# Kernel tuning notes

Measured on AMD Instinct MI355X. Metric: run time of the kernel, lower is better.

Reference implementation:

```python
import jax, jax.numpy as jnp
import numpy as np

H = 2048   # hidden_size
NH = 16    # num_heads
D = 128    # head_dim_qk == head_dim_v
K = 4      # conv_kernel_size


def _causal_depthwise_conv(x, w, b):
    # x: [B,S,C], w: [C,K], b: [C]. Matches torch Conv1d(groups=C, padding=K-1)[..., :S]
    S = x.shape[1]
    xp = jnp.pad(x, ((0, 0), (K - 1, 0), (0, 0)))
    y = b
    for j in range(K):
        y = y + xp[:, j:j + S, :] * w[:, j]
    return y


def setup_inputs() -> dict:
    key = jax.random.key(0)
    ks = jax.random.split(key, 18)
    s = 0.02
    B, S = 2, 2048
    return {
        "x": jax.random.normal(ks[0], (B, S, H), dtype=jnp.float32),
        "Wq": jax.random.normal(ks[1], (H, NH * D), dtype=jnp.float32) * s,
        "Wk": jax.random.normal(ks[2], (H, NH * D), dtype=jnp.float32) * s,
        "Wv": jax.random.normal(ks[3], (H, NH * D), dtype=jnp.float32) * s,
        "Wa": jax.random.normal(ks[4], (H, NH), dtype=jnp.float32) * s,
        "ba": jax.random.normal(ks[5], (NH,), dtype=jnp.float32) * s,
        "Wb": jax.random.normal(ks[6], (H, NH), dtype=jnp.float32) * s,
        "bb": jax.random.normal(ks[7], (NH,), dtype=jnp.float32) * s,
        "Wg": jax.random.normal(ks[8], (H, NH * D), dtype=jnp.float32) * s,
        "Wo": jax.random.normal(ks[9], (NH * D, H), dtype=jnp.float32) * s,
        "qcw": jax.random.normal(ks[10], (NH * D, K), dtype=jnp.float32) * s,
        "qcb": jax.random.normal(ks[11], (NH * D,), dtype=jnp.float32) * s,
        "kcw": jax.random.normal(ks[12], (NH * D, K), dtype=jnp.float32) * s,
        "kcb": jax.random.normal(ks[13], (NH * D,), dtype=jnp.float32) * s,
        "vcw": jax.random.normal(ks[14], (NH * D, K), dtype=jnp.float32) * s,
        "vcb": jax.random.normal(ks[15], (NH * D,), dtype=jnp.float32) * s,
        "ln_w": jnp.ones((D,), dtype=jnp.float32),
        "ln_b": jnp.zeros((D,), dtype=jnp.float32),
    }


def _forward(x, Wq, Wk, Wv, Wa, ba, Wb, bb, Wg, Wo,
             qcw, qcb, kcw, kcb, vcw, vcb, ln_w, ln_b):
    B, S, _ = x.shape
    q = _causal_depthwise_conv(x @ Wq, qcw, qcb)
    k = _causal_depthwise_conv(x @ Wk, kcw, kcb)
    v = _causal_depthwise_conv(x @ Wv, vcw, vcb)
    q = jax.nn.silu(q).reshape(B, S, NH, D)
    k = jax.nn.silu(k).reshape(B, S, NH, D) * (D ** -0.5)
    v = jax.nn.silu(v).reshape(B, S, NH, D)
    alpha = jax.nn.sigmoid(x @ Wa + ba)  # [B,S,NH]
    beta = jax.nn.sigmoid(x @ Wb + bb)   # [B,S,NH]

    # time-major for scan
    qt = jnp.moveaxis(q, 1, 0)       # [S,B,NH,D]
    kt = jnp.moveaxis(k, 1, 0)
    vt = jnp.moveaxis(v, 1, 0)
    at = jnp.moveaxis(alpha, 1, 0)   # [S,B,NH]
    bt = jnp.moveaxis(beta, 1, 0)

    def step(St, inp):
        q_, k_, v_, a_, b_ = inp
        sk = jnp.einsum('bhij,bhj->bhi', St, k_)            # [B,NH,D]
        err = sk - v_
        Sn = (a_[..., None, None] * St
              - b_[..., None, None] * err[..., None] * k_[..., None, :])
        o_ = jnp.einsum('bhij,bhj->bhi', Sn, q_)
        return Sn, o_

    S0 = jnp.zeros((B, NH, D, D), dtype=x.dtype)
    _, o = jax.lax.scan(step, S0, (qt, kt, vt, at, bt))
    o = jnp.moveaxis(o, 0, 1)  # [B,S,NH,D]

    # LayerNorm over head_dim
    mu = jnp.mean(o, axis=-1, keepdims=True)
    var = jnp.mean(jnp.square(o - mu), axis=-1, keepdims=True)
    o = (o - mu) * jax.lax.rsqrt(var + 1e-5) * ln_w + ln_b

    g = jax.nn.sigmoid(x @ Wg).reshape(B, S, NH, D)
    o = (o * g).reshape(B, S, NH * D)
    return o @ Wo


def reference(x, Wq, Wk, Wv, Wa, ba, Wb, bb, Wg, Wo,
              qcw, qcb, kcw, kcb, vcw, vcb, ln_w, ln_b):
    return _forward(x, Wq, Wk, Wv, Wa, ba, Wb, bb, Wg, Wo,
                    qcw, qcb, kcw, kcb, vcw, vcb, ln_w, ln_b)
```

## Files before the change

### kernel.cpp

```cpp
#include <hip/hip_runtime.h>
#include <math.h>
#include <stdint.h>

typedef unsigned short u16;
typedef unsigned int u32;
typedef __attribute__((ext_vector_type(8))) short short8;
typedef __attribute__((ext_vector_type(4))) float f32x4;

#define MFMA16(a, b, c) __builtin_amdgcn_mfma_f32_16x16x32_bf16(a, b, c, 0, 0, 0)

__device__ __forceinline__ u16 f2bf(float f) {
  union { float f; u32 u; } v; v.f = f;
  return (u16)((v.u + 0x7FFFu + ((v.u >> 16) & 1u)) >> 16);
}
__device__ __forceinline__ float bf2f(u16 h) {
  union { u32 u; float f; } v; v.u = ((u32)h) << 16; return v.f;
}
__device__ __forceinline__ float bflo(u32 p) {
  union { u32 u; float f; } v; v.u = p << 16; return v.f;
}
__device__ __forceinline__ float bfhi(u32 p) {
  union { u32 u; float f; } v; v.u = p & 0xffff0000u; return v.f;
}
__device__ __forceinline__ float sigm(float x) { return 1.f / (1.f + expf(-x)); }

__global__ void k_cvt_x(const float* __restrict__ x, u16* __restrict__ xb) {
  int i = (blockIdx.x * 256 + threadIdx.x) * 8;
  float4 a = *(const float4*)(x + i);
  float4 b = *(const float4*)(x + i + 4);
  uint4 p;
  p.x = (u32)f2bf(a.x) | ((u32)f2bf(a.y) << 16);
  p.y = (u32)f2bf(a.z) | ((u32)f2bf(a.w) << 16);
  p.z = (u32)f2bf(b.x) | ((u32)f2bf(b.y) << 16);
  p.w = (u32)f2bf(b.z) | ((u32)f2bf(b.w) << 16);
  *(uint4*)(xb + i) = p;
}

__global__ void k_tconv(const float* __restrict__ W, u16* __restrict__ Wt) {
  __shared__ float tile[32][33];
  int n0 = blockIdx.x * 32, k0 = blockIdx.y * 32;
  int tc = threadIdx.x & 31, tr = threadIdx.x >> 5;
  #pragma unroll
  for (int p = 0; p < 4; ++p) {
    int k = k0 + p * 8 + tr;
    tile[p * 8 + tr][tc] = W[(size_t)k * 2048 + n0 + tc];
  }
  __syncthreads();
  #pragma unroll
  for (int p = 0; p < 4; ++p) {
    int n = n0 + p * 8 + tr;
    Wt[(size_t)n * 2048 + k0 + tc] = f2bf(tile[tc][p * 8 + tr]);
  }
}

__global__ void k_tconv4(const float* __restrict__ W0, const float* __restrict__ W1,
                         const float* __restrict__ W2, const float* __restrict__ W3,
                         u16* __restrict__ Wt) {
  __shared__ float tile[32][33];
  int z = blockIdx.z;
  const float* W = (z == 0) ? W0 : (z == 1) ? W1 : (z == 2) ? W2 : W3;
  u16* dst = Wt + (size_t)z * 2048 * 2048;
  int n0 = blockIdx.x * 32, k0 = blockIdx.y * 32;
  int tc = threadIdx.x & 31, tr = threadIdx.x >> 5;
  #pragma unroll
  for (int p = 0; p < 4; ++p) {
    int k = k0 + p * 8 + tr;
    tile[p * 8 + tr][tc] = W[(size_t)k * 2048 + n0 + tc];
  }
  __syncthreads();
  #pragma unroll
  for (int p = 0; p < 4; ++p) {
    int n = n0 + p * 8 + tr;
    dst[(size_t)n * 2048 + k0 + tc] = f2bf(tile[tc][p * 8 + tr]);
  }
}

__device__ __forceinline__ void gld_lds16(const u16* g, u16* l) {
  __builtin_amdgcn_global_load_lds((const __attribute__((address_space(1))) void*)g,
                                   (__attribute__((address_space(3))) void*)l, 16, 0, 0);
}

template <int MODE>
__global__ void k_gemm(const u16* __restrict__ A, const u16* __restrict__ Bw,
                       void* C0, void* C1, int Kd) {
  __shared__ u16 As[2][128 * 32];
  __shared__ u16 Bs[2][128 * 32];
  const int t = threadIdx.x;
  const int lane = t & 63, wv = t >> 6;
  const int wr = wv >> 1, wc = wv & 1;
  const int m0 = blockIdx.y * 128, n0 = blockIdx.x * 128;
  f32x4 acc[4][4] = {};
  const int NT = Kd / 32;

  auto stage = [&](int buf, int kt) {
    #pragma unroll
    for (int i = 0; i < 2; ++i) {
      int li = i * 256 + t;
      int row = li >> 2, kc = li & 3;
      const u16* ga = A + (size_t)(m0 + row) * Kd + kt * 32 + kc * 8;
      gld_lds16(ga, &As[buf][(i * 256 + wv * 64) * 8]);
      const u16* gb = Bw + (size_t)(n0 + row) * Kd + kt * 32 + kc * 8;
      gld_lds16(gb, &Bs[buf][(i * 256 + wv * 64) * 8]);
    }
  };

  stage(0, 0);
  __syncthreads();
  int buf = 0;
  const int l15 = lane & 15, l4 = lane >> 4;
  for (int kt = 0; kt < NT; ++kt) {
    if (kt + 1 < NT) stage(buf ^ 1, kt + 1);
    short8 af[4], bfr[4];
    #pragma unroll
    for (int m = 0; m < 4; ++m)
      af[m] = *(const short8*)&As[buf][(wr * 64 + m * 16 + l15) * 32 + l4 * 8];
    #pragma unroll
    for (int n = 0; n < 4; ++n)
      bfr[n] = *(const short8*)&Bs[buf][(wc * 64 + n * 16 + l15) * 32 + l4 * 8];
    #pragma unroll
    for (int m = 0; m < 4; ++m)
      #pragma unroll
      for (int n = 0; n < 4; ++n)
        acc[m][n] = MFMA16(af[m], bfr[n], acc[m][n]);
    __syncthreads();
    buf ^= 1;
  }
  #pragma unroll
  for (int m = 0; m < 4; ++m)
    #pragma unroll
    for (int n = 0; n < 4; ++n)
      #pragma unroll
      for (int e = 0; e < 4; ++e) {
        int row = m0 + wr * 64 + m * 16 + l4 * 4 + e;
        int col = n0 + wc * 64 + n * 16 + l15;
        if (MODE == 0) {
          ((float*)C0)[(size_t)row * 2048 + col] = acc[m][n][e];
        } else {
          u16 vb = f2bf(acc[m][n][e]);
          if (n0 < 6144) ((u16*)C0)[(size_t)row * 6144 + col] = vb;
          else           ((u16*)C1)[(size_t)row * 2048 + (col - 6144)] = vb;
        }
      }
}

template <int MODE>
__global__ __launch_bounds__(512)
void k_gemm8(const u16* __restrict__ A, const u16* __restrict__ Bw,
             void* C0, void* C1) {
  __shared__ u16 lds[65536];
  const int t = threadIdx.x;
  const int w = t >> 6, lane = t & 63;
  const int l15 = lane & 15, l4 = lane >> 4;
  const int wm = w >> 2, wn = w & 3;
  const int m0 = blockIdx.y * 256, n0 = blockIdx.x * 256;

  f32x4 acc[8][4] = {};
  short8 a[4][2], b[4][2];

  auto stageHalf = [&](int buf, int kt, int mat, int half) {
    const u16* src = mat ? Bw : A;
    const int row0 = (mat ? n0 : m0) + half * 128;
    u16* dst0 = &lds[mat * 32768 + (buf * 2 + half) * 8192 + w * 1024];
    #pragma unroll
    for (int i = 0; i < 2; ++i) {
      int f = w * 128 + i * 64 + lane;
      int rr = f >> 3, g = f & 7;
      const u16* ga = src + (size_t)(row0 + rr) * 2048 + kt * 64 + ((g ^ (rr & 7)) << 3);
      gld_lds16(ga, dst0 + i * 512);
    }
  };
  auto rdA = [&](int buf, int mq, int ks) {
    int row = wm * 64 + (mq & 3) * 16 + l15;
    int g = (l4 + ks * 4) ^ (row & 7);
    return *(const short8*)&lds[(buf * 2 + (mq >> 2)) * 8192 + row * 64 + g * 8];
  };
  auto rdB = [&](int buf, int n, int ks) {
    int row = wn * 32 + (n & 1) * 16 + l15;
    int g = (l4 + ks * 4) ^ (row & 7);
    return *(const short8*)&lds[32768 + (buf * 2 + (n >> 1)) * 8192 + row * 64 + g * 8];
  };

  stageHalf(0, 0, 0, 0); stageHalf(0, 0, 1, 0);
  stageHalf(0, 0, 1, 1); stageHalf(0, 0, 0, 1);
  asm volatile("s_waitcnt vmcnt(0)" ::: "memory");
  __builtin_amdgcn_s_barrier();
  __builtin_amdgcn_sched_barrier(0);

  for (int kt = 0; kt < 32; ++kt) {
    const int bufc = kt & 1, bufn = bufc ^ 1;
    const int ktn = (kt + 1 < 32) ? kt + 1 : 31;

    #pragma unroll
    for (int mq = 0; mq < 4; ++mq) { a[mq][0] = rdA(bufc, mq, 0); a[mq][1] = rdA(bufc, mq, 1); }
    #pragma unroll
    for (int n = 0; n < 2; ++n) { b[n][0] = rdB(bufc, n, 0); b[n][1] = rdB(bufc, n, 1); }
    stageHalf(bufn, ktn, 0, 0);
    __builtin_amdgcn_s_barrier();
    asm volatile("s_waitcnt lgkmcnt(0)" ::: "memory");
    __builtin_amdgcn_sched_barrier(0);
    __builtin_amdgcn_s_setprio(1);
    #pragma unroll
    for (int mq = 0; mq < 4; ++mq)
      #pragma unroll
      for (int n = 0; n < 2; ++n) {
        acc[mq][n] = MFMA16(a[mq][0], b[n][0], acc[mq][n]);
        acc[mq][n] = MFMA16(a[mq][1], b[n][1], acc[mq][n]);
      }
    __builtin_amdgcn_s_setprio(0);
    asm volatile("s_waitcnt vmcnt(4)" ::: "memory");
    __builtin_amdgcn_s_barrier();
    __builtin_amdgcn_sched_barrier(0);

    #pragma unroll
    for (int n = 2; n < 4; ++n) { b[n][0] = rdB(bufc, n, 0); b[n][1] = rdB(bufc, n, 1); }
    stageHalf(bufn, ktn, 1, 0);
    __builtin_amdgcn_s_barrier();
    asm volatile("s_waitcnt lgkmcnt(0)" ::: "memory");
    __builtin_amdgcn_sched_barrier(0);
    __builtin_amdgcn_s_setprio(1);
    #pragma unroll
    for (int mq = 0; mq < 4; ++mq)
      #pragma unroll
      for (int n = 2; n < 4; ++n) {
        acc[mq][n] = MFMA16(a[mq][0], b[n][0], acc[mq][n]);
        acc[mq][n] = MFMA16(a[mq][1], b[n][1], acc[mq][n]);
      }
    __builtin_amdgcn_s_setprio(0);
    asm volatile("s_waitcnt vmcnt(4)" ::: "memory");
    __builtin_amdgcn_s_barrier();
    __builtin_amdgcn_sched_barrier(0);

    #pragma unroll
    for (int mq = 0; mq < 4; ++mq) { a[mq][0] = rdA(bufc, mq + 4, 0); a[mq][1] = rdA(bufc, mq + 4, 1); }
    stageHalf(bufn, ktn, 1, 1);
    __builtin_amdgcn_s_barrier();
    asm volatile("s_waitcnt lgkmcnt(0)" ::: "memory");
    __builtin_amdgcn_sched_barrier(0);
    __builtin_amdgcn_s_setprio(1);
    #pragma unroll
    for (int mq = 0; mq < 4; ++mq)
      #pragma unroll
      for (int n = 2; n < 4; ++n) {
        acc[mq + 4][n] = MFMA16(a[mq][0], b[n][0], acc[mq + 4][n]);
        acc[mq + 4][n] = MFMA16(a[mq][1], b[n][1], acc[mq + 4][n]);
      }
    __builtin_amdgcn_s_setprio(0);
    __builtin_amdgcn_s_barrier();
    __builtin_amdgcn_sched_barrier(0);

    stageHalf(bufn, ktn, 0, 1);
    __builtin_amdgcn_s_barrier();
    asm volatile("s_waitcnt lgkmcnt(0)" ::: "memory");
    __builtin_amdgcn_sched_barrier(0);
    __builtin_amdgcn_s_setprio(1);
    #pragma unroll
    for (int mq = 0; mq < 4; ++mq)
      #pragma unroll
      for (int n = 0; n < 2; ++n) {
        acc[mq + 4][n] = MFMA16(a[mq][0], b[n][0], acc[mq + 4][n]);
        acc[mq + 4][n] = MFMA16(a[mq][1], b[n][1], acc[mq + 4][n]);
      }
    __builtin_amdgcn_s_setprio(0);
    asm volatile("s_waitcnt vmcnt(4)" ::: "memory");
    __builtin_amdgcn_s_barrier();
    __builtin_amdgcn_sched_barrier(0);
  }

  const bool toG = (MODE == 1) && (n0 >= 6144);
  #pragma unroll
  for (int mq = 0; mq < 8; ++mq) {
    int row = m0 + (mq >> 2) * 128 + wm * 64 + (mq & 3) * 16 + l4 * 4;
    #pragma unroll
    for (int n = 0; n < 4; ++n) {
      int col = n0 + (n >> 1) * 128 + wn * 32 + (n & 1) * 16 + l15;
      #pragma unroll
      for (int e = 0; e < 4; ++e) {
        if (MODE == 0) {
          ((float*)C0)[(size_t)(row + e) * 2048 + col] = acc[mq][n][e];
        } else {
          u16 vb = f2bf(acc[mq][n][e]);
          if (!toG) ((u16*)C0)[(size_t)(row + e) * 6144 + col] = vb;
          else      ((u16*)C1)[(size_t)(row + e) * 2048 + (col - 6144)] = vb;
        }
      }
    }
  }
}

__global__ void k_ab(const float* __restrict__ x, const float* __restrict__ Wa,
                     const float* __restrict__ ba, const float* __restrict__ Wb,
                     const float* __restrict__ bb, float* __restrict__ ab2) {
  int t = threadIdx.x;
  int col = t & 31, lr = t >> 5;
  int rowi = blockIdx.x * 8 + lr;
  const float* W = (col < 16) ? Wa : Wb;
  int c = col & 15;
  float acc = 0.f;
  const float* xr = x + (size_t)rowi * 2048;
  for (int k = 0; k < 2048; k += 4) {
    float4 xv = *(const float4*)(xr + k);
    acc += xv.x * W[(k + 0) * 16 + c] + xv.y * W[(k + 1) * 16 + c] +
           xv.z * W[(k + 2) * 16 + c] + xv.w * W[(k + 3) * 16 + c];
  }
  acc += (col < 16) ? ba[c] : bb[c];
  float sg = sigm(acc);
  int b = rowi >> 11, s = rowi & 2047;
  size_t base = ((size_t)(b * 16 + c) * 2048 + s) * 2;
  if (col < 16) ab2[base + 0] = sg;
  else          ab2[base + 1] = sg;
}

__global__ void k_conv(const u16* __restrict__ projQKV,
                       const float* __restrict__ qcw, const float* __restrict__ qcb,
                       const float* __restrict__ kcw, const float* __restrict__ kcb,
                       const float* __restrict__ vcw, const float* __restrict__ vcb,
                       u16* __restrict__ qkv2) {
  int idx = blockIdx.x * 256 + threadIdx.x;
  int cq = idx % 1536, rrow = idx / 1536;
  int c = cq * 4;
  int s = rrow & 2047, b = rrow >> 11;
  int type = c >> 11;
  int ch = c & 2047;
  int h = ch >> 7, d = ch & 127;
  const float* cw; const float* cb;
  if (type == 0)      { cw = qcw; cb = qcb; }
  else if (type == 1) { cw = kcw; cb = kcb; }
  else                { cw = vcw; cb = vcb; }
  float wch[4][4];
  #pragma unroll
  for (int u = 0; u < 4; ++u) {
    float4 wv = *(const float4*)(cw + (ch + u) * 4);
    wch[u][0] = wv.x; wch[u][1] = wv.y; wch[u][2] = wv.z; wch[u][3] = wv.w;
  }
  float4 bv = *(const float4*)(cb + ch);
  float accv[4] = {bv.x, bv.y, bv.z, bv.w};
  #pragma unroll
  for (int j = 0; j < 4; ++j) {
    int sj = s - 3 + j;
    if (sj < 0) continue;
    const u16* p = projQKV + (size_t)(rrow + j - 3) * 6144 + c;
    u32 pa = *(const u32*)p;
    u32 pb = *(const u32*)(p + 2);
    accv[0] += bflo(pa) * wch[0][j];
    accv[1] += bfhi(pa) * wch[1][j];
    accv[2] += bflo(pb) * wch[2][j];
    accv[3] += bfhi(pb) * wch[3][j];
  }
  u16 o4[4];
  #pragma unroll
  for (int u = 0; u < 4; ++u) {
    float y = accv[u];
    float sv = y * sigm(y);
    if (type == 1) sv *= 0.08838834764831845f;
    o4[u] = f2bf(sv);
  }
  int off = (type == 1 ? 0 : (type == 0 ? 128 : 256)) + d;
  u16* dst = qkv2 + ((size_t)(b * 16 + h) * 2048 + s) * 384 + off;
  *(u32*)dst       = (u32)o4[0] | ((u32)o4[1] << 16);
  *(u32*)(dst + 2) = (u32)o4[2] | ((u32)o4[3] << 16);
}

__global__ __launch_bounds__(256)
void k_chunkA(const u16* __restrict__ qkv2, const float* __restrict__ ab2,
              u16* __restrict__ Tbv, u16* __restrict__ nTbk,
              u16* __restrict__ Aq, float* __restrict__ vecs,
              u16* __restrict__ Kt) {
  __shared__ u16 Kl[64][136], Ql[64][136];
  __shared__ float Gk[4096], Gq[4096];
  __shared__ float clL[64], laL[64], bL[64], gpL[64];
  const int unit = blockIdx.x;
  const int bh = unit >> 5, c = unit & 31;
  const int t = threadIdx.x;
  const int wv = t >> 6, lane = t & 63;
  const int l15 = lane & 15, l4 = lane >> 4;
  const u16* qb = qkv2 + ((size_t)bh * 2048 + c * 64) * 384;

  #pragma unroll
  for (int p = 0; p < 4; ++p) {
    int ld = p * 256 + t;
    int row = ld >> 4, c8 = (ld & 15) * 8;
    *(uint4*)&Kl[row][c8] = *(const uint4*)(qb + (size_t)row * 384 + c8);
    *(uint4*)&Ql[row][c8] = *(const uint4*)(qb + (size_t)row * 384 + 128 + c8);
  }
  if (wv == 0) {
    float2 abv = *(const float2*)(ab2 + ((size_t)bh * 2048 + c * 64 + lane) * 2);
    float la = log2f(abv.x);
    float cl = la;
    #pragma unroll
    for (int o = 1; o < 64; o <<= 1) {
      float nv = __shfl_up(cl, o, 64);
      if (lane >= o) cl += nv;
    }
    clL[lane] = cl; laL[lane] = la; bL[lane] = abv.y;
    gpL[lane] = exp2f(cl - la);
  }
  __syncthreads();

  {
    const int t0 = (wv >> 1) * 32, i0 = (wv & 1) * 32;
    f32x4 ak[2][2] = {}, aq[2][2] = {};
    #pragma unroll
    for (int ks = 0; ks < 4; ++ks) {
      short8 bk[2], Ka[2], Qa[2];
      #pragma unroll
      for (int n = 0; n < 2; ++n)
        bk[n] = *(const short8*)&Kl[i0 + n * 16 + l15][ks * 32 + l4 * 8];
      #pragma unroll
      for (int m = 0; m < 2; ++m) {
        Ka[m] = *(const short8*)&Kl[t0 + m * 16 + l15][ks * 32 + l4 * 8];
        Qa[m] = *(const short8*)&Ql[t0 + m * 16 + l15][ks * 32 + l4 * 8];
      }
      #pragma unroll
      for (int m = 0; m < 2; ++m)
        #pragma unroll
        for (int n = 0; n < 2; ++n) {
          ak[m][n] = MFMA16(Ka[m], bk[n], ak[m][n]);
          aq[m][n] = MFMA16(Qa[m], bk[n], aq[m][n]);
        }
    }
    #pragma unroll
    for (int m = 0; m < 2; ++m)
      #pragma unroll
      for (int n = 0; n < 2; ++n)
        #pragma unroll
        for (int e = 0; e < 4; ++e) {
          int row = t0 + m * 16 + l4 * 4 + e;
          int col = i0 + n * 16 + l15;
          Gk[row * 64 + col] = ak[m][n][e];
          Gq[row * 64 + col] = aq[m][n][e];
        }
  }
  __syncthreads();

  #pragma unroll
  for (int p = 0; p < 16; ++p) {
    int e = p * 256 + t; int tt = e >> 6, ii = e & 63;
    float lv = 0.f;
    if (ii < tt) lv = bL[tt] * Gk[e] * exp2f(clL[tt] - laL[tt] - clL[ii]);
    float av = (ii <= tt) ? Gq[e] * exp2f(clL[tt] - clL[ii]) : 0.f;
    Gk[e] = lv;
    Aq[(size_t)unit * 4096 + e] = f2bf(av);
  }
  __syncthreads();

  float X[64];
  if (t < 128) {
    #pragma unroll
    for (int r = 0; r < 64; ++r)
      X[r] = bL[r] * bf2f(qb[(size_t)r * 384 + 256 + t]);
  } else {
    int ck = t - 128;
    #pragma unroll
    for (int r = 0; r < 64; ++r)
      X[r] = -bL[r] * gpL[r] * bf2f(Kl[r][ck]);
  }
  #pragma unroll
  for (int i = 0; i < 63; ++i) {
    float xi = X[i];
    #pragma unroll
    for (int r = i + 1; r < 64; ++r)
      X[r] = fmaf(-Gk[r * 64 + i], xi, X[r]);
  }
  if (t < 128) {
    #pragma unroll
    for (int r = 0; r < 64; ++r)
      Tbv[(size_t)unit * 8192 + r * 128 + t] = f2bf(X[r]);
  } else {
    #pragma unroll
    for (int r = 0; r < 64; ++r)
      nTbk[(size_t)unit * 8192 + r * 128 + (t - 128)] = f2bf(X[r]);
  }
  if (t < 64) {
    vecs[(size_t)unit * 128 + t] = exp2f(clL[t]);
    vecs[(size_t)unit * 128 + 64 + t] = exp2f(clL[63] - clL[t]);
  }
  {
    int dk = t >> 1, tt0 = (t & 1) * 32;
    uint4 w[4];
    u16* wp = (u16*)w;
    #pragma unroll
    for (int j = 0; j < 32; ++j) wp[j] = Kl[tt0 + j][dk];
    uint4* dst = (uint4*)(Kt + (size_t)unit * 8192 + dk * 64 + tt0);
    dst[0] = w[0]; dst[1] = w[1]; dst[2] = w[2]; dst[3] = w[3];
  }
}

#define OFF_NT  0
#define OFF_AQ  8192
#define OFF_Q   12288
#define OFF_KT  20480
#define OFF_TBV 28672
#define STG_U16 29696

__global__ __launch_bounds__(256)
void k_chunkB(const u16* __restrict__ qkv2, const u16* __restrict__ Tbv,
              const u16* __restrict__ nTbk, const u16* __restrict__ Aq,
              const u16* __restrict__ Kt, const float* __restrict__ vecs,
              float* __restrict__ o) {
  __shared__ u16 stg[2][STG_U16];
  __shared__ float S[16 * 132];
  __shared__ u16 Ut[16 * 72], Utd[16 * 72];
  __shared__ float gdl[2][128];
  const int bid = blockIdx.x;
  const int xcd = bid & 7, within = bid >> 3;
  const int sl = within & 7, hgrp = within >> 3;
  const int bh = hgrp * 8 + xcd;
  const int dv0 = sl * 16;
  const int b = bh >> 4, h = bh & 15;
  const int t = threadIdx.x;
  const int wv = t >> 6, lane = t & 63;
  const int l15 = lane & 15, l4 = lane >> 4;
  const int t0 = wv * 16;
  const int dk0 = wv * 32;
  const u16* qbase = qkv2 + (size_t)bh * 2048 * 384;
  float* obase = o + (size_t)b * 2048 * 2048 + h * 128 + dv0;

  for (int p = t; p < 16 * 132; p += 256) S[p] = 0.f;

  auto stage = [&](int buf, int c) {
    u16* sb = &stg[buf][0];
    const size_t unit = (size_t)bh * 32 + c;
    const u16* tbk = nTbk + unit * 8192;
    const u16* aqp = Aq + unit * 4096;
    const u16* ktp = Kt + unit * 8192;
    const u16* tbv = Tbv + unit * 8192;
    const u16* qp  = qbase + (size_t)c * 64 * 384 + 128;
    #pragma unroll
    for (int r = 0; r < 4; ++r) {
      int f = r * 256 + t; int rr = f >> 4, c16 = f & 15;
      gld_lds16(tbk + rr * 128 + (c16 ^ (rr & 7)) * 8, sb + OFF_NT + (r * 256 + wv * 64) * 8);
    }
    #pragma unroll
    for (int r = 0; r < 2; ++r) {
      int f = r * 256 + t; int rr = f >> 3, c8 = f & 7;
      gld_lds16(aqp + rr * 64 + (c8 ^ (rr & 7)) * 8, sb + OFF_AQ + (r * 256 + wv * 64) * 8);
    }
    #pragma unroll
    for (int r = 0; r < 4; ++r) {
      int f = r * 256 + t; int rr = f >> 4, c16 = f & 15;
      gld_lds16(qp + rr * 384 + (c16 ^ (rr & 7)) * 8, sb + OFF_Q + (r * 256 + wv * 64) * 8);
    }
    #pragma unroll
    for (int r = 0; r < 4; ++r) {
      int f = r * 256 + t; int rr = f >> 3, c8 = f & 7;
      gld_lds16(ktp + rr * 64 + (c8 ^ (rr & 7)) * 8, sb + OFF_KT + (r * 256 + wv * 64) * 8);
    }
    if (t < 128)
      gld_lds16(tbv + (t >> 1) * 128 + dv0 + (t & 1) * 8, sb + OFF_TBV + wv * 64 * 8);
  };

  stage(0, 0);
  if (t < 128) gdl[0][t] = vecs[(size_t)bh * 32 * 128 + t];
  __syncthreads();

  for (int c = 0; c < 32; ++c) {
    const int buf = c & 1;
    const u16* sb = &stg[buf][0];
    float vnext = 0.f;
    if (c + 1 < 32) {
      stage(buf ^ 1, c + 1);
      if (t < 128) vnext = vecs[((size_t)bh * 32 + c + 1) * 128 + t];
    }

    f32x4 acc1 = {}, acc2 = {};
    #pragma unroll
    for (int e = 0; e < 4; ++e)
      acc1[e] = bf2f(sb[OFF_TBV + (t0 + l4 * 4 + e) * 16 + l15]);
    #pragma unroll
    for (int ks = 0; ks < 4; ++ks) {
      short8 bhi, blo;
      {
        const float* srow = &S[l15 * 132 + ks * 32 + l4 * 8];
        float4 s0 = *(const float4*)srow, s1 = *(const float4*)(srow + 4);
        float sv[8] = {s0.x, s0.y, s0.z, s0.w, s1.x, s1.y, s1.z, s1.w};
        #pragma unroll
        for (int j = 0; j < 8; ++j) {
          u16 hv = f2bf(sv[j]);
          bhi[j] = (short)hv;
          blo[j] = (short)f2bf(sv[j] - bf2f(hv));
        }
      }
      const int cx = ((ks * 4 + l4) ^ (l15 & 7)) * 8;
      short8 a1 = *(const short8*)&sb[OFF_NT + (t0 + l15) * 128 + cx];
      short8 a2 = *(const short8*)&sb[OFF_Q + (t0 + l15) * 128 + cx];
      acc1 = MFMA16(a1, bhi, acc1);
      acc1 = MFMA16(a1, blo, acc1);
      acc2 = MFMA16(a2, bhi, acc2);
      acc2 = MFMA16(a2, blo, acc2);
    }
    {
      u16 up[4], ud[4];
      #pragma unroll
      for (int e = 0; e < 4; ++e) {
        float uv = acc1[e];
        up[e] = f2bf(uv);
        ud[e] = f2bf(uv * gdl[buf][64 + t0 + l4 * 4 + e]);
      }
      int ux = l15 * 72 + t0 + l4 * 4;
      *(u32*)&Ut[ux]      = (u32)up[0] | ((u32)up[1] << 16);
      *(u32*)&Ut[ux + 2]  = (u32)up[2] | ((u32)up[3] << 16);
      *(u32*)&Utd[ux]     = (u32)ud[0] | ((u32)ud[1] << 16);
      *(u32*)&Utd[ux + 2] = (u32)ud[2] | ((u32)ud[3] << 16);
    }
    asm volatile("s_waitcnt lgkmcnt(0)" ::: "memory");
    __builtin_amdgcn_s_barrier();
    __builtin_amdgcn_sched_barrier(0);

    #pragma unroll
    for (int e = 0; e < 4; ++e) acc2[e] *= gdl[buf][t0 + l4 * 4 + e];
    #pragma unroll
    for (int ks = 0; ks < 2; ++ks) {
      const int cx = ((ks * 4 + l4) ^ (l15 & 7)) * 8;
      short8 af = *(const short8*)&sb[OFF_AQ + (t0 + l15) * 64 + cx];
      short8 bf_ = *(const short8*)&Ut[l15 * 72 + ks * 32 + l4 * 8];
      acc2 = MFMA16(af, bf_, acc2);
    }
    #pragma unroll
    for (int e = 0; e < 4; ++e)
      obase[(size_t)(c * 64 + t0 + l4 * 4 + e) * 2048 + l15] = acc2[e];

    f32x4 acc3[2] = {};
    #pragma unroll
    for (int ks = 0; ks < 2; ++ks) {
      short8 a3 = *(const short8*)&Utd[l15 * 72 + ks * 32 + l4 * 8];
      #pragma unroll
      for (int n = 0; n < 2; ++n) {
        const int kr = dk0 + n * 16 + l15;
        const int cx = ((ks * 4 + l4) ^ (l15 & 7)) * 8;
        short8 b3 = *(const short8*)&sb[OFF_KT + kr * 64 + cx];
        acc3[n] = MFMA16(a3, b3, acc3[n]);
      }
    }
    float gtot = gdl[buf][63];
    #pragma unroll
    for (int n = 0; n < 2; ++n)
      #pragma unroll
      for (int e = 0; e < 4; ++e) {
        float* sp = &S[(l4 * 4 + e) * 132 + dk0 + n * 16 + l15];
        *sp = gtot * *sp + acc3[n][e];
      }
    if (c + 1 < 32 && t < 128) gdl[buf ^ 1][t] = vnext;
    __syncthreads();
  }
}

__global__ void k_lng(const float* __restrict__ o, const u16* __restrict__ projG,
                      const float* __restrict__ ln_w, const float* __restrict__ ln_b,
                      u16* __restrict__ og) {
  int gidx = blockIdx.x * 4 + (threadIdx.x >> 6);
  int lane = threadIdx.x & 63;
  int rrow = gidx >> 4, h = gidx & 15;
  const float* op = o + (size_t)rrow * 2048 + h * 128;
  float2 x2 = *(const float2*)(op + lane * 2);
  float sum = x2.x + x2.y, sq = x2.x * x2.x + x2.y * x2.y;
  #pragma unroll
  for (int m = 1; m < 64; m <<= 1) {
    sum += __shfl_xor(sum, m, 64);
    sq  += __shfl_xor(sq, m, 64);
  }
  float mu = sum * (1.f / 128.f);
  float var = sq * (1.f / 128.f) - mu * mu;
  float rs = 1.0f / sqrtf(var + 1e-5f);
  u32 gu = *(const u32*)(projG + (size_t)rrow * 2048 + h * 128 + lane * 2);
  float g0 = sigm(bflo(gu)), g1 = sigm(bfhi(gu));
  int d0 = lane * 2;
  float y0 = ((x2.x - mu) * rs * ln_w[d0] + ln_b[d0]) * g0;
  float y1 = ((x2.y - mu) * rs * ln_w[d0 + 1] + ln_b[d0 + 1]) * g1;
  *(u32*)(og + (size_t)rrow * 2048 + h * 128 + d0) = (u32)f2bf(y0) | ((u32)f2bf(y1) << 16);
}

extern "C" void kernel_launch(void* const* d_in, const int* in_sizes, int n_in,
                              void* d_out, int out_size, void* d_ws, size_t ws_size,
                              hipStream_t stream) {
  const float* x   = (const float*)d_in[0];
  const float* Wq  = (const float*)d_in[1];
  const float* Wk  = (const float*)d_in[2];
  const float* Wv  = (const float*)d_in[3];
  const float* Wa  = (const float*)d_in[4];
  const float* ba  = (const float*)d_in[5];
  const float* Wb  = (const float*)d_in[6];
  const float* bb  = (const float*)d_in[7];
  const float* Wg  = (const float*)d_in[8];
  const float* Wo  = (const float*)d_in[9];
  const float* qcw = (const float*)d_in[10];
  const float* qcb = (const float*)d_in[11];
  const float* kcw = (const float*)d_in[12];
  const float* kcb = (const float*)d_in[13];
  const float* vcw = (const float*)d_in[14];
  const float* vcb = (const float*)d_in[15];
  const float* lnw = (const float*)d_in[16];
  const float* lnb = (const float*)d_in[17];
  float* out = (float*)d_out;

  if (ws_size < 168820736ull) return;
  char* ws = (char*)d_ws;
  u16*   xb   = (u16*)(ws);
  u16*   Kt   = (u16*)(ws);
  u16*   og   = (u16*)(ws);
  u16*   Wt   = (u16*)(ws + 16777216);
  u16*   Wot  = (u16*)(ws + 16777216);
  u16*   Tbv  = (u16*)(ws + 25165824);
  u16*   Aq   = (u16*)(ws + 41943040);
  u16*   pQKV = (u16*)(ws + 50331648);
  float* oB   = (float*)(ws + 50331648);
  u16*   nTbk = (u16*)(ws + 83886080);
  u16*   pG   = (u16*)(ws + 100663296);
  u16*   qkv2 = (u16*)(ws + 117440512);
  float* ab2  = (float*)(ws + 167772160);
  float* vecs = (float*)(ws + 168296448);

  k_cvt_x<<<4096, 256, 0, stream>>>(x, xb);
  k_tconv4<<<dim3(64, 64, 4), 256, 0, stream>>>(Wq, Wk, Wv, Wg, Wt);
  k_ab<<<512, 256, 0, stream>>>(x, Wa, ba, Wb, bb, ab2);

  k_gemm8<1><<<dim3(32, 16), 512, 0, stream>>>(xb, Wt, pQKV, pG);
  k_tconv<<<dim3(64, 64), 256, 0, stream>>>(Wo, Wot);
  k_conv<<<24576, 256, 0, stream>>>(pQKV, qcw, qcb, kcw, kcb, vcw, vcb, qkv2);
  k_chunkA<<<1024, 256, 0, stream>>>(qkv2, ab2, Tbv, nTbk, Aq, vecs, Kt);
  k_chunkB<<<256, 256, 0, stream>>>(qkv2, Tbv, nTbk, Aq, Kt, vecs, oB);
  k_lng<<<16384, 256, 0, stream>>>(oB, pG, lnw, lnb, og);
  k_gemm<0><<<dim3(16, 32), 256, 0, stream>>>(og, Wot, out, nullptr, 2048);
}
```

Baseline: 483.3 us.

## Merge prep kernels, swizzle small-GEMM LDS, and remap big-GEMM block order

Three separate prep kernels (x conversion, weight transpose, alpha/beta projection) become one launch that picks its work by block index, saving launch gaps and letting the pieces overlap. The 128x128 output GEMM now XOR-swizzles its LDS k-chunks to cut bank conflicts on fragment reads. The projection GEMM moves to a 1D grid with a remapped tile order so that blocks running together share more A/B tiles in L2. The fused prep kernel has uneven per-block work, with the alpha/beta blocks much heavier than the others, which can leave a slow tail.

```diff
diff --git a/kernel.cpp b/kernel.cpp
--- a/kernel.cpp
+++ b/kernel.cpp
@@ -24,16 +24,65 @@
 }
 __device__ __forceinline__ float sigm(float x) { return 1.f / (1.f + expf(-x)); }
 
-__global__ void k_cvt_x(const float* __restrict__ x, u16* __restrict__ xb) {
-  int i = (blockIdx.x * 256 + threadIdx.x) * 8;
-  float4 a = *(const float4*)(x + i);
-  float4 b = *(const float4*)(x + i + 4);
-  uint4 p;
-  p.x = (u32)f2bf(a.x) | ((u32)f2bf(a.y) << 16);
-  p.y = (u32)f2bf(a.z) | ((u32)f2bf(a.w) << 16);
-  p.z = (u32)f2bf(b.x) | ((u32)f2bf(b.y) << 16);
-  p.w = (u32)f2bf(b.z) | ((u32)f2bf(b.w) << 16);
-  *(uint4*)(xb + i) = p;
+__global__ __launch_bounds__(256)
+void k_prep(const float* __restrict__ x, u16* __restrict__ xb,
+            const float* __restrict__ Wq, const float* __restrict__ Wk,
+            const float* __restrict__ Wv, const float* __restrict__ Wg,
+            u16* __restrict__ Wt,
+            const float* __restrict__ Wa, const float* __restrict__ ba,
+            const float* __restrict__ Wb, const float* __restrict__ bb,
+            float* __restrict__ ab2) {
+  __shared__ float tile[32][33];
+  const int bid = blockIdx.x;
+  if (bid < 4096) {
+    int i = (bid * 256 + threadIdx.x) * 8;
+    float4 a = *(const float4*)(x + i);
+    float4 b = *(const float4*)(x + i + 4);
+    uint4 p;
+    p.x = (u32)f2bf(a.x) | ((u32)f2bf(a.y) << 16);
+    p.y = (u32)f2bf(a.z) | ((u32)f2bf(a.w) << 16);
+    p.z = (u32)f2bf(b.x) | ((u32)f2bf(b.y) << 16);
+    p.w = (u32)f2bf(b.z) | ((u32)f2bf(b.w) << 16);
+    *(uint4*)(xb + i) = p;
+  } else if (bid < 20480) {
+    int zz = bid - 4096;
+    int z = zz >> 12, rest = zz & 4095;
+    int bx = rest & 63, by = rest >> 6;
+    const float* W = (z == 0) ? Wq : (z == 1) ? Wk : (z == 2) ? Wv : Wg;
+    u16* dst = Wt + (size_t)z * 2048 * 2048;
+    int n0 = bx * 32, k0 = by * 32;
+    int tc = threadIdx.x & 31, tr = threadIdx.x >> 5;
+    #pragma unroll
+    for (int p = 0; p < 4; ++p) {
+      int k = k0 + p * 8 + tr;
+      tile[p * 8 + tr][tc] = W[(size_t)k * 2048 + n0 + tc];
+    }
+    __syncthreads();
+    #pragma unroll
+    for (int p = 0; p < 4; ++p) {
+      int n = n0 + p * 8 + tr;
+      dst[(size_t)n * 2048 + k0 + tc] = f2bf(tile[tc][p * 8 + tr]);
+    }
+  } else {
+    int t = threadIdx.x;
+    int col = t & 31, lr = t >> 5;
+    int rowi = (bid - 20480) * 8 + lr;
+    const float* W = (col < 16) ? Wa : Wb;
+    int c = col & 15;
+    float acc = 0.f;
+    const float* xr = x + (size_t)rowi * 2048;
+    for (int k = 0; k < 2048; k += 4) {
+      float4 xv = *(const float4*)(xr + k);
+      acc += xv.x * W[(k + 0) * 16 + c] + xv.y * W[(k + 1) * 16 + c] +
+             xv.z * W[(k + 2) * 16 + c] + xv.w * W[(k + 3) * 16 + c];
+    }
+    acc += (col < 16) ? ba[c] : bb[c];
+    float sg = sigm(acc);
+    int b = rowi >> 11, s = rowi & 2047;
+    size_t base = ((size_t)(b * 16 + c) * 2048 + s) * 2;
+    if (col < 16) ab2[base + 0] = sg;
+    else          ab2[base + 1] = sg;
+  }
 }
 
 __global__ void k_tconv(const float* __restrict__ W, u16* __restrict__ Wt) {
@@ -50,28 +99,6 @@
   for (int p = 0; p < 4; ++p) {
     int n = n0 + p * 8 + tr;
     Wt[(size_t)n * 2048 + k0 + tc] = f2bf(tile[tc][p * 8 + tr]);
-  }
-}
-
-__global__ void k_tconv4(const float* __restrict__ W0, const float* __restrict__ W1,
-                         const float* __restrict__ W2, const float* __restrict__ W3,
-                         u16* __restrict__ Wt) {
-  __shared__ float tile[32][33];
-  int z = blockIdx.z;
-  const float* W = (z == 0) ? W0 : (z == 1) ? W1 : (z == 2) ? W2 : W3;
-  u16* dst = Wt + (size_t)z * 2048 * 2048;
-  int n0 = blockIdx.x * 32, k0 = blockIdx.y * 32;
-  int tc = threadIdx.x & 31, tr = threadIdx.x >> 5;
-  #pragma unroll
-  for (int p = 0; p < 4; ++p) {
-    int k = k0 + p * 8 + tr;
-    tile[p * 8 + tr][tc] = W[(size_t)k * 2048 + n0 + tc];
-  }
-  __syncthreads();
-  #pragma unroll
-  for (int p = 0; p < 4; ++p) {
-    int n = n0 + p * 8 + tr;
-    dst[(size_t)n * 2048 + k0 + tc] = f2bf(tile[tc][p * 8 + tr]);
   }
 }
 
@@ -97,9 +124,10 @@
     for (int i = 0; i < 2; ++i) {
       int li = i * 256 + t;
       int row = li >> 2, kc = li & 3;
-      const u16* ga = A + (size_t)(m0 + row) * Kd + kt * 32 + kc * 8;
+      int kcs = kc ^ ((row >> 1) & 3);
+      const u16* ga = A + (size_t)(m0 + row) * Kd + kt * 32 + kcs * 8;
       gld_lds16(ga, &As[buf][(i * 256 + wv * 64) * 8]);
-      const u16* gb = Bw + (size_t)(n0 + row) * Kd + kt * 32 + kc * 8;
+      const u16* gb = Bw + (size_t)(n0 + row) * Kd + kt * 32 + kcs * 8;
       gld_lds16(gb, &Bs[buf][(i * 256 + wv * 64) * 8]);
     }
   };
@@ -112,11 +140,17 @@
     if (kt + 1 < NT) stage(buf ^ 1, kt + 1);
     short8 af[4], bfr[4];
     #pragma unroll
-    for (int m = 0; m < 4; ++m)
-      af[m] = *(const short8*)&As[buf][(wr * 64 + m * 16 + l15) * 32 + l4 * 8];
-    #pragma unroll
-    for (int n = 0; n < 4; ++n)
-      bfr[n] = *(const short8*)&Bs[buf][(wc * 64 + n * 16 + l15) * 32 + l4 * 8];
+    for (int m = 0; m < 4; ++m) {
+      int row = wr * 64 + m * 16 + l15;
+      int g = l4 ^ ((row >> 1) & 3);
+      af[m] = *(const short8*)&As[buf][row * 32 + g * 8];
+    }
+    #pragma unroll
+    for (int n = 0; n < 4; ++n) {
+      int row = wc * 64 + n * 16 + l15;
+      int g = l4 ^ ((row >> 1) & 3);
+      bfr[n] = *(const short8*)&Bs[buf][row * 32 + g * 8];
+    }
     #pragma unroll
     for (int m = 0; m < 4; ++m)
       #pragma unroll
@@ -152,7 +186,10 @@
   const int w = t >> 6, lane = t & 63;
   const int l15 = lane & 15, l4 = lane >> 4;
   const int wm = w >> 2, wn = w & 3;
-  const int m0 = blockIdx.y * 256, n0 = blockIdx.x * 256;
+  const int bid = blockIdx.x;
+  const int mt = ((bid & 7) << 1) | ((bid >> 3) & 1);
+  const int nt = bid >> 4;
+  const int m0 = mt * 256, n0 = nt * 256;
 
   f32x4 acc[8][4] = {};
   short8 a[4][2], b[4][2];
@@ -285,29 +322,6 @@
       }
     }
   }
-}
-
-__global__ void k_ab(const float* __restrict__ x, const float* __restrict__ Wa,
-                     const float* __restrict__ ba, const float* __restrict__ Wb,
-                     const float* __restrict__ bb, float* __restrict__ ab2) {
-  int t = threadIdx.x;
-  int col = t & 31, lr = t >> 5;
-  int rowi = blockIdx.x * 8 + lr;
-  const float* W = (col < 16) ? Wa : Wb;
-  int c = col & 15;
-  float acc = 0.f;
-  const float* xr = x + (size_t)rowi * 2048;
-  for (int k = 0; k < 2048; k += 4) {
-    float4 xv = *(const float4*)(xr + k);
-    acc += xv.x * W[(k + 0) * 16 + c] + xv.y * W[(k + 1) * 16 + c] +
-           xv.z * W[(k + 2) * 16 + c] + xv.w * W[(k + 3) * 16 + c];
-  }
-  acc += (col < 16) ? ba[c] : bb[c];
-  float sg = sigm(acc);
-  int b = rowi >> 11, s = rowi & 2047;
-  size_t base = ((size_t)(b * 16 + c) * 2048 + s) * 2;
-  if (col < 16) ab2[base + 0] = sg;
-  else          ab2[base + 1] = sg;
 }
 
 __global__ void k_conv(const u16* __restrict__ projQKV,
@@ -709,11 +723,8 @@
   float* ab2  = (float*)(ws + 167772160);
   float* vecs = (float*)(ws + 168296448);
 
-  k_cvt_x<<<4096, 256, 0, stream>>>(x, xb);
-  k_tconv4<<<dim3(64, 64, 4), 256, 0, stream>>>(Wq, Wk, Wv, Wg, Wt);
-  k_ab<<<512, 256, 0, stream>>>(x, Wa, ba, Wb, bb, ab2);
-
-  k_gemm8<1><<<dim3(32, 16), 512, 0, stream>>>(xb, Wt, pQKV, pG);
+  k_prep<<<20992, 256, 0, stream>>>(x, xb, Wq, Wk, Wv, Wg, Wt, Wa, ba, Wb, bb, ab2);
+  k_gemm8<1><<<512, 512, 0, stream>>>(xb, Wt, pQKV, pG);
   k_tconv<<<dim3(64, 64), 256, 0, stream>>>(Wo, Wot);
   k_conv<<<24576, 256, 0, stream>>>(pQKV, qcw, qcb, kcw, kcb, vcw, vcb, qkv2);
   k_chunkA<<<1024, 256, 0, stream>>>(qkv2, ab2, Tbv, nTbk, Aq, vecs, Kt);
```

Measured after the change: 674.4 us. 39.5% more time.

## Tile k_ab through LDS, swizzle k_gemm LDS, remap k_gemm8 block order

Applied to the files above, without the earlier changes.

Rewrites the alpha/beta projection kernel to stage x rows and the Wa/Wb slices in shared memory per 128-wide K tile, instead of each thread streaming its whole x row and strided weight loads from global memory. Adds an XOR swizzle to the LDS layout of the generic k_gemm so fragment reads avoid bank conflicts. Remaps the k_gemm8 grid to a 1D launch with an interleaved M-tile order so neighbouring blocks share B tiles in cache. The k_ab rewrite adds two barriers per K tile.

```diff
diff --git a/kernel.cpp b/kernel.cpp
--- a/kernel.cpp
+++ b/kernel.cpp
@@ -36,23 +36,6 @@
   *(uint4*)(xb + i) = p;
 }
 
-__global__ void k_tconv(const float* __restrict__ W, u16* __restrict__ Wt) {
-  __shared__ float tile[32][33];
-  int n0 = blockIdx.x * 32, k0 = blockIdx.y * 32;
-  int tc = threadIdx.x & 31, tr = threadIdx.x >> 5;
-  #pragma unroll
-  for (int p = 0; p < 4; ++p) {
-    int k = k0 + p * 8 + tr;
-    tile[p * 8 + tr][tc] = W[(size_t)k * 2048 + n0 + tc];
-  }
-  __syncthreads();
-  #pragma unroll
-  for (int p = 0; p < 4; ++p) {
-    int n = n0 + p * 8 + tr;
-    Wt[(size_t)n * 2048 + k0 + tc] = f2bf(tile[tc][p * 8 + tr]);
-  }
-}
-
 __global__ void k_tconv4(const float* __restrict__ W0, const float* __restrict__ W1,
                          const float* __restrict__ W2, const float* __restrict__ W3,
                          u16* __restrict__ Wt) {
@@ -73,6 +56,68 @@
     int n = n0 + p * 8 + tr;
     dst[(size_t)n * 2048 + k0 + tc] = f2bf(tile[tc][p * 8 + tr]);
   }
+}
+
+__global__ void k_tconv(const float* __restrict__ W, u16* __restrict__ Wt) {
+  __shared__ float tile[32][33];
+  int n0 = blockIdx.x * 32, k0 = blockIdx.y * 32;
+  int tc = threadIdx.x & 31, tr = threadIdx.x >> 5;
+  #pragma unroll
+  for (int p = 0; p < 4; ++p) {
+    int k = k0 + p * 8 + tr;
+    tile[p * 8 + tr][tc] = W[(size_t)k * 2048 + n0 + tc];
+  }
+  __syncthreads();
+  #pragma unroll
+  for (int p = 0; p < 4; ++p) {
+    int n = n0 + p * 8 + tr;
+    Wt[(size_t)n * 2048 + k0 + tc] = f2bf(tile[tc][p * 8 + tr]);
+  }
+}
+
+__global__ __launch_bounds__(256)
+void k_ab(const float* __restrict__ x, const float* __restrict__ Wa,
+          const float* __restrict__ ba, const float* __restrict__ Wb,
+          const float* __restrict__ bb, float* __restrict__ ab2) {
+  __shared__ float Wl[128 * 32];
+  __shared__ float xl[8][128];
+  const int t = threadIdx.x;
+  const int lr = t >> 5, c = t & 31;
+  const int r0 = blockIdx.x * 8;
+  const int ch = c & 15;
+  const float* Wsrc = (c < 16) ? Wa : Wb;
+  float acc = 0.f;
+  for (int kt = 0; kt < 16; ++kt) {
+    #pragma unroll
+    for (int i = 0; i < 16; ++i) {
+      int idx = i * 256 + t;
+      int kk = idx >> 5, cc = idx & 31;
+      const float* Ws = (cc < 16) ? Wa : Wb;
+      Wl[kk * 32 + cc] = Ws[(kt * 128 + kk) * 16 + (cc & 15)];
+    }
+    #pragma unroll
+    for (int i = 0; i < 4; ++i) {
+      int idx = i * 256 + t;
+      int rr = idx >> 7, kk = idx & 127;
+      xl[rr][kk] = x[(size_t)(r0 + rr) * 2048 + kt * 128 + kk];
+    }
+    __syncthreads();
+    #pragma unroll
+    for (int kk = 0; kk < 128; kk += 4) {
+      float2 x01 = *(const float2*)&xl[lr][kk];
+      float2 x23 = *(const float2*)&xl[lr][kk + 2];
+      acc += x01.x * Wl[(kk + 0) * 32 + c] + x01.y * Wl[(kk + 1) * 32 + c]
+           + x23.x * Wl[(kk + 2) * 32 + c] + x23.y * Wl[(kk + 3) * 32 + c];
+    }
+    __syncthreads();
+  }
+  acc += (c < 16) ? ba[ch] : bb[ch];
+  float sg = sigm(acc);
+  int rowi = r0 + lr;
+  int b = rowi >> 11, s = rowi & 2047;
+  size_t base = ((size_t)(b * 16 + ch) * 2048 + s) * 2;
+  if (c < 16) ab2[base + 0] = sg;
+  else        ab2[base + 1] = sg;
 }
 
 __device__ __forceinline__ void gld_lds16(const u16* g, u16* l) {
@@ -97,9 +142,10 @@
     for (int i = 0; i < 2; ++i) {
       int li = i * 256 + t;
       int row = li >> 2, kc = li & 3;
-      const u16* ga = A + (size_t)(m0 + row) * Kd + kt * 32 + kc * 8;
+      int kcs = kc ^ ((row >> 1) & 3);
+      const u16* ga = A + (size_t)(m0 + row) * Kd + kt * 32 + kcs * 8;
       gld_lds16(ga, &As[buf][(i * 256 + wv * 64) * 8]);
-      const u16* gb = Bw + (size_t)(n0 + row) * Kd + kt * 32 + kc * 8;
+      const u16* gb = Bw + (size_t)(n0 + row) * Kd + kt * 32 + kcs * 8;
       gld_lds16(gb, &Bs[buf][(i * 256 + wv * 64) * 8]);
     }
   };
@@ -112,11 +158,17 @@
     if (kt + 1 < NT) stage(buf ^ 1, kt + 1);
     short8 af[4], bfr[4];
     #pragma unroll
-    for (int m = 0; m < 4; ++m)
-      af[m] = *(const short8*)&As[buf][(wr * 64 + m * 16 + l15) * 32 + l4 * 8];
-    #pragma unroll
-    for (int n = 0; n < 4; ++n)
-      bfr[n] = *(const short8*)&Bs[buf][(wc * 64 + n * 16 + l15) * 32 + l4 * 8];
+    for (int m = 0; m < 4; ++m) {
+      int row = wr * 64 + m * 16 + l15;
+      int g = l4 ^ ((row >> 1) & 3);
+      af[m] = *(const short8*)&As[buf][row * 32 + g * 8];
+    }
+    #pragma unroll
+    for (int n = 0; n < 4; ++n) {
+      int row = wc * 64 + n * 16 + l15;
+      int g = l4 ^ ((row >> 1) & 3);
+      bfr[n] = *(const short8*)&Bs[buf][row * 32 + g * 8];
+    }
     #pragma unroll
     for (int m = 0; m < 4; ++m)
       #pragma unroll
@@ -152,7 +204,10 @@
   const int w = t >> 6, lane = t & 63;
   const int l15 = lane & 15, l4 = lane >> 4;
   const int wm = w >> 2, wn = w & 3;
-  const int m0 = blockIdx.y * 256, n0 = blockIdx.x * 256;
+  const int bid = blockIdx.x;
+  const int mt = ((bid & 7) << 1) | ((bid >> 3) & 1);
+  const int nt = bid >> 4;
+  const int m0 = mt * 256, n0 = nt * 256;
 
   f32x4 acc[8][4] = {};
   short8 a[4][2], b[4][2];
@@ -285,29 +340,6 @@
       }
     }
   }
-}
-
-__global__ void k_ab(const float* __restrict__ x, const float* __restrict__ Wa,
-                     const float* __restrict__ ba, const float* __restrict__ Wb,
-                     const float* __restrict__ bb, float* __restrict__ ab2) {
-  int t = threadIdx.x;
-  int col = t & 31, lr = t >> 5;
-  int rowi = blockIdx.x * 8 + lr;
-  const float* W = (col < 16) ? Wa : Wb;
-  int c = col & 15;
-  float acc = 0.f;
-  const float* xr = x + (size_t)rowi * 2048;
-  for (int k = 0; k < 2048; k += 4) {
-    float4 xv = *(const float4*)(xr + k);
-    acc += xv.x * W[(k + 0) * 16 + c] + xv.y * W[(k + 1) * 16 + c] +
-           xv.z * W[(k + 2) * 16 + c] + xv.w * W[(k + 3) * 16 + c];
-  }
-  acc += (col < 16) ? ba[c] : bb[c];
-  float sg = sigm(acc);
-  int b = rowi >> 11, s = rowi & 2047;
-  size_t base = ((size_t)(b * 16 + c) * 2048 + s) * 2;
-  if (col < 16) ab2[base + 0] = sg;
-  else          ab2[base + 1] = sg;
 }
 
 __global__ void k_conv(const u16* __restrict__ projQKV,
@@ -713,7 +745,7 @@
   k_tconv4<<<dim3(64, 64, 4), 256, 0, stream>>>(Wq, Wk, Wv, Wg, Wt);
   k_ab<<<512, 256, 0, stream>>>(x, Wa, ba, Wb, bb, ab2);
 
-  k_gemm8<1><<<dim3(32, 16), 512, 0, stream>>>(xb, Wt, pQKV, pG);
+  k_gemm8<1><<<512, 512, 0, stream>>>(xb, Wt, pQKV, pG);
   k_tconv<<<dim3(64, 64), 256, 0, stream>>>(Wo, Wot);
   k_conv<<<24576, 256, 0, stream>>>(pQKV, qcw, qcb, kcw, kcb, vcw, vcb, qkv2);
   k_chunkA<<<1024, 256, 0, stream>>>(qkv2, ab2, Tbv, nTbk, Aq, vecs, Kt);
```

Result: faster. 466.9 us (-3.4%).
